# Performance work log

Hardware: AMD Instinct MI355X
Metric: run time of the kernel (lower is better)

## Reference

```python
import jax, jax.numpy as jnp
import numpy as np

B, T, H, V = 16, 400, 400, 22000
S, STEPS, NG = 30, 8, 3  # n_slots, max_res_len, n_gates


def setup_inputs() -> dict:
    key = jax.random.key(0)
    ks = jax.random.split(key, 12)
    r = lambda k, shape, s: jax.random.normal(k, shape, jnp.float32) * s
    lens = jnp.sort(jax.random.randint(ks[8], (B,), T // 2, T + 1))[::-1]
    lens = lens.at[0].set(T)  # torch code only masks up to max(lens); make max(lens)==T
    return {
        "embedding": r(ks[0], (V, H), 0.1),
        "gru_Wih": r(ks[1], (3 * H, H), 0.05),
        "gru_Whh": r(ks[2], (3 * H, H), 0.05),
        "gru_bih": jnp.zeros((3 * H,), jnp.float32),
        "gru_bhh": jnp.zeros((3 * H,), jnp.float32),
        "W_ratio": r(ks[3], (1, 3 * H), 0.05),
        "b_ratio": jnp.zeros((1,), jnp.float32),
        "W_gate": r(ks[4], (NG, H), 0.05),
        "b_gate": jnp.zeros((NG,), jnp.float32),
        "slot_embs": r(ks[5], (S, H), 0.1),  # domain_emb + slot_emb, precombined per domain-slot
        "encoded_hidden": r(ks[6], (B, H), 1.0),
        "encoded_outputs": r(ks[7], (B, T, H), 1.0),
        "encoded_lens": lens,
        "story": jax.random.randint(ks[9], (B, T), 0, V),
        "target_batches": jax.random.randint(ks[10], (B, S, STEPS), 0, V),
    }


def reference(embedding, gru_Wih, gru_Whh, gru_bih, gru_bhh, W_ratio, b_ratio,
              W_gate, b_gate, slot_embs, encoded_hidden, encoded_outputs,
              encoded_lens, story, target_batches):
    # dropout is identity at eval; use_teacher_forcing=True.
    mask = jnp.arange(T)[None, :] < encoded_lens[:, None]          # [B, T]
    batch_idx = jnp.arange(B)[:, None]

    def gru_cell(x, h):
        gi = x @ gru_Wih.T + gru_bih                                # [B, 3H]
        gh = h @ gru_Whh.T + gru_bhh
        i_r, i_z, i_n = jnp.split(gi, 3, axis=-1)
        h_r, h_z, h_n = jnp.split(gh, 3, axis=-1)
        r = jax.nn.sigmoid(i_r + h_r)
        z = jax.nn.sigmoid(i_z + h_z)
        n = jnp.tanh(i_n + r * h_n)
        return (1.0 - z) * n + z * h

    def per_slot(slot_emb, tgt_steps):  # slot_emb [H], tgt_steps [STEPS, B]
        dec_in0 = jnp.broadcast_to(slot_emb[None, :], (B, H))

        def step(carry, tgt_w):
            h, dec_in = carry
            h = gru_cell(dec_in, h)                                 # dec_state == new hidden
            logits = jnp.einsum('bth,bh->bt', encoded_outputs, h)   # [B, T]
            attn = jax.nn.softmax(jnp.where(mask, logits, -1e9), axis=1)
            context = jnp.einsum('bt,bth->bh', attn, encoded_outputs)
            p_vocab = jax.nn.softmax(h @ embedding.T, axis=1)       # [B, V]
            pg_in = jnp.concatenate([h, context, dec_in], axis=-1)  # [B, 3H]
            p_gen = jax.nn.sigmoid(pg_in @ W_ratio.T + b_ratio)     # [B, 1]
            p_ctx = jnp.zeros((B, V), p_vocab.dtype).at[batch_idx, story].add(attn)
            p_final = (1.0 - p_gen) * p_ctx + p_gen * p_vocab       # [B, V]
            dec_next = embedding[tgt_w]                             # teacher forcing
            return (h, dec_next), (p_final, context)

        _, (points, contexts) = jax.lax.scan(step, (encoded_hidden, dec_in0), tgt_steps)
        gate = contexts[0] @ W_gate.T + b_gate                      # gate uses step-0 context
        return jnp.transpose(points, (1, 0, 2)), gate               # [B, STEPS, V], [B, NG]

    targets = jnp.transpose(target_batches, (1, 2, 0))              # [S, STEPS, B]
    all_point_outputs, all_gate_outputs = jax.vmap(per_slot)(slot_embs, targets)
    return all_point_outputs, all_gate_outputs  # [S,B,STEPS,V], [S,B,NG]
```

## Files before the change

### kernel.cpp

```cpp
#include <hip/hip_runtime.h>
#include <hip/hip_bf16.h>

#define DEV __device__ __forceinline__

constexpr int B = 16, T = 400, H = 400, V = 22000, S = 30, STEPS = 8, NG = 3;
constexpr int M  = S * B;
constexpr int H3 = 3 * H;
constexpr int KP = 416;
constexpr int VP = 22016;
constexpr int MP = 512;
constexpr int MR = STEPS * MP;
constexpr int NWP = 1280;
constexpr int NBLK = VP / 128;
constexpr int NMP = MR / 256;
constexpr int NVB = NBLK * NMP;
constexpr int NVB_S = NBLK * 2;
constexpr int NCT = (H3 + 63) / 64;
constexpr int NGH = NCT * ((M + 63) / 64);
constexpr int TPAD = 416;
constexpr int PLD = 424;
constexpr long long PTS = (long long)S * B * STEPS * V;

typedef __attribute__((ext_vector_type(8))) short bfrag;
typedef __attribute__((ext_vector_type(4))) float f32x4;
typedef unsigned short u16;

DEV u16 f2bf(float x) {
  unsigned u = __float_as_uint(x);
  u += 0x7FFFu + ((u >> 16) & 1u);
  return (u16)(u >> 16);
}
DEV u16 f2bfn(float x) {
  __hip_bfloat16 h = __float2bfloat16(x);
  union { __hip_bfloat16 b; u16 u; } cv; cv.b = h; return cv.u;
}
DEV float bf2f(u16 h) { return __uint_as_float(((unsigned)h) << 16); }
DEV float sigm(float x) { return 1.0f / (1.0f + __expf(-x)); }

DEV void gload16(const u16* g, u16* l) {
  __builtin_amdgcn_global_load_lds(
      (const __attribute__((address_space(1))) void*)g,
      (__attribute__((address_space(3))) void*)l, 16, 0, 0);
}

constexpr int N_EMB = VP * KP / 256;
constexpr int N_ENC = B * 400 * TPAD / 256;
constexpr int N_W   = NWP * KP / 256;
constexpr int N_DEC = STEPS * MP * KP / 256;
constexpr int N_H0  = MP * KP / 256;
constexpr int N_ZP  = STEPS * (MP - M) * KP / 256;
constexpr int N_ZE  = MR * 16 / 256;
constexpr int N_INIT = N_EMB + N_ENC + N_W + N_DEC + N_H0 + N_ZP + N_ZE;

__global__ __launch_bounds__(256) void k_init(
    const float* __restrict__ emb, const float* __restrict__ enc,
    const float* __restrict__ Wih, const float* __restrict__ Whh,
    const float* __restrict__ semb, const float* __restrict__ ehid,
    const int* __restrict__ tgt,
    u16* __restrict__ ebf, u16* __restrict__ encbK, u16* __restrict__ encT,
    u16* __restrict__ wihH, u16* __restrict__ wihL,
    u16* __restrict__ whhH, u16* __restrict__ whhL,
    float* __restrict__ dec, u16* __restrict__ decH, u16* __restrict__ decL,
    float* __restrict__ h0F, u16* __restrict__ h0H, u16* __restrict__ h0L,
    u16* __restrict__ hAllH, u16* __restrict__ hAllL, u16* __restrict__ ebuf)
{
  int bx = blockIdx.x;
  const int tid = threadIdx.x;
  if (bx < N_EMB) {
    int i = bx * 256 + tid;
    int v = i / KP, k = i % KP;
    ebf[i] = f2bf((v < V && k < H) ? emb[(long long)v * H + k] : 0.f);
    return;
  }
  bx -= N_EMB;
  if (bx < N_ENC) {
    int i = bx * 256 + tid;
    int c = i % TPAD, r = (i / TPAD) % 400, b = i / (TPAD * 400);
    encbK[i] = f2bf((c < H) ? enc[((size_t)b * T + r) * H + c] : 0.f);
    encT[i]  = f2bf((c < T) ? enc[((size_t)b * T + c) * H + r] : 0.f);
    return;
  }
  bx -= N_ENC;
  if (bx < N_W) {
    int i = bx * 256 + tid;
    int n = i / KP, k = i % KP;
    float v1 = (n < H3 && k < H) ? Wih[n * H + k] : 0.f;
    u16 h1 = f2bf(v1);
    wihH[i] = h1; wihL[i] = f2bf(v1 - bf2f(h1));
    float v2 = (n < H3 && k < H) ? Whh[n * H + k] : 0.f;
    u16 h2 = f2bf(v2);
    whhH[i] = h2; whhL[i] = f2bf(v2 - bf2f(h2));
    return;
  }
  bx -= N_W;
  if (bx < N_DEC) {
    int i = bx * 256 + tid;
    int k = i % KP, m = (i / KP) % MP, s = i / (KP * MP);
    float val = 0.f;
    if (m < M && k < H) {
      int slot = m / B, b = m % B;
      if (s == 0) val = semb[slot * H + k];
      else        val = emb[(long long)tgt[(b * S + slot) * STEPS + (s - 1)] * H + k];
      dec[((long long)s * M + m) * H + k] = val;
    }
    u16 hi = f2bf(val);
    decH[i] = hi; decL[i] = f2bf(val - bf2f(hi));
    return;
  }
  bx -= N_DEC;
  if (bx < N_H0) {
    int i = bx * 256 + tid;
    int k = i % KP, m = i / KP;
    float val = (m < M && k < H) ? ehid[(m % B) * H + k] : 0.f;
    if (m < M && k < H) h0F[m * H + k] = val;
    u16 hi = f2bf(val);
    h0H[i] = hi; h0L[i] = f2bf(val - bf2f(hi));
    return;
  }
  bx -= N_H0;
  if (bx < N_ZP) {
    int i = bx * 256 + tid;
    int k = i % KP;
    int row = M + (i / KP) % (MP - M);
    int s = i / (KP * (MP - M));
    size_t idx = ((size_t)s * MP + row) * KP + k;
    hAllH[idx] = 0; hAllL[idx] = 0;
    return;
  }
  bx -= N_ZP;
  {
    int i = bx * 256 + tid;
    int row = i / 16, col = V + (i % 16);
    ebuf[(size_t)row * VP + col] = 0;
  }
}

__global__ __launch_bounds__(256) void k_gemm64s(
    const u16* __restrict__ Ahi, const u16* __restrict__ Alo,
    const u16* __restrict__ Bmh, const u16* __restrict__ Bml,
    const float* __restrict__ bias, float* __restrict__ C,
    int Mvalid, int Nvalid, int Cstride)
{
  __shared__ u16 BsH[64 * 32], BsL[64 * 32];
  const int tid = threadIdx.x;
  const int wave = tid >> 6, lane = tid & 63;
  const int wm = wave >> 1, wn = wave & 1;
  const int n0 = blockIdx.x * 64;
  const int m0 = blockIdx.y * 64;
  const int lrow = lane & 15;
  const int c16 = lane >> 4;
  const int srow = tid >> 2;
  const int sg = (tid & 3) ^ (srow & 3);
  f32x4 acc[2][2] = {};

  const u16* aH = Ahi + (size_t)(m0 + wm * 32 + lrow) * KP + c16 * 8;
  const u16* aL = Alo + (size_t)(m0 + wm * 32 + lrow) * KP + c16 * 8;
  const u16* bHs = Bmh + (size_t)(n0 + srow) * KP + sg * 8;
  const u16* bLs = Bml + (size_t)(n0 + srow) * KP + sg * 8;
  u16* lBH = BsH + wave * 512;
  u16* lBL = BsL + wave * 512;

  for (int kk = 0; kk < KP / 32; ++kk) {
    const int kb = kk * 32;
    gload16(bHs + kb, lBH);
    gload16(bLs + kb, lBL);
    __syncthreads();
    bfrag a0h = *(const bfrag*)(aH + kb);
    bfrag a1h = *(const bfrag*)(aH + 16 * KP + kb);
    bfrag a0l = *(const bfrag*)(aL + kb);
    bfrag a1l = *(const bfrag*)(aL + 16 * KP + kb);
#pragma unroll
    for (int nn = 0; nn < 2; ++nn) {
      const int br = wn * 32 + nn * 16 + lrow;
      const int goff = br * 32 + ((c16 ^ (br & 3)) << 3);
      bfrag bh = *(const bfrag*)&BsH[goff];
      bfrag bl = *(const bfrag*)&BsL[goff];
      acc[0][nn] = __builtin_amdgcn_mfma_f32_16x16x32_bf16(a0h, bh, acc[0][nn], 0, 0, 0);
      acc[1][nn] = __builtin_amdgcn_mfma_f32_16x16x32_bf16(a1h, bh, acc[1][nn], 0, 0, 0);
      acc[0][nn] = __builtin_amdgcn_mfma_f32_16x16x32_bf16(a0h, bl, acc[0][nn], 0, 0, 0);
      acc[1][nn] = __builtin_amdgcn_mfma_f32_16x16x32_bf16(a1h, bl, acc[1][nn], 0, 0, 0);
      acc[0][nn] = __builtin_amdgcn_mfma_f32_16x16x32_bf16(a0l, bh, acc[0][nn], 0, 0, 0);
      acc[1][nn] = __builtin_amdgcn_mfma_f32_16x16x32_bf16(a1l, bh, acc[1][nn], 0, 0, 0);
    }
    __syncthreads();
  }
  const int orow = (lane >> 4) << 2, ocol = lane & 15;
#pragma unroll
  for (int am = 0; am < 2; ++am) {
#pragma unroll
    for (int nn = 0; nn < 2; ++nn) {
      const int gn = n0 + wn * 32 + nn * 16 + ocol;
      if (gn >= Nvalid) continue;
      const float badd = bias[gn];
#pragma unroll
      for (int r = 0; r < 4; ++r) {
        const int gm = m0 + wm * 32 + am * 16 + orow + r;
        if (gm < Mvalid) C[(long long)gm * Cstride + gn] = acc[am][nn][r] + badd;
      }
    }
  }
}

__global__ __launch_bounds__(512) void k_cell(const float* __restrict__ gi_s,
                                              const float* __restrict__ gh,
                                              const float* __restrict__ hprevF,
                                              float* __restrict__ hcurF,
                                              u16* __restrict__ hHc, u16* __restrict__ hLc) {
  int i = blockIdx.x * 512 + threadIdx.x;
  if (i >= M * H) return;
  int k = i % H, m = i / H;
  float ir = gi_s[m * H3 + k],         hr = gh[m * H3 + k];
  float iz = gi_s[m * H3 + H + k],     hz = gh[m * H3 + H + k];
  float in_ = gi_s[m * H3 + 2*H + k],  hn = gh[m * H3 + 2*H + k];
  float rr = sigm(ir + hr);
  float z = sigm(iz + hz);
  float n = tanhf(in_ + rr * hn);
  float hv = (1.f - z) * n + z * hprevF[i];
  hcurF[i] = hv;
  u16 hb = f2bf(hv);
  hHc[m * KP + k] = hb;
  hLc[m * KP + k] = f2bf(hv - bf2f(hb));
}

__global__ __launch_bounds__(512) void k_bigv(
    const u16* __restrict__ hPrevH, const u16* __restrict__ hPrevL,
    const u16* __restrict__ ebf, u16* __restrict__ ebuf, long long Rbase,
    const u16* __restrict__ whhH, const u16* __restrict__ whhL,
    const float* __restrict__ bhh, float* __restrict__ gh)
{
  __shared__ union SMU {
    u16 vb[4][4096];
    struct { u16 bh[64 * 32]; u16 bl[64 * 32]; } g;
  } sm;
  const int bx = blockIdx.x;
  const int tid = threadIdx.x;
  const int wave = tid >> 6, lane = tid & 63;

  if (bx < NVB_S) {
    const int bxs = (bx & 7) * (NVB_S / 8) + (bx >> 3);
    const int nb = bxs >> 1;
    const int m0 = (bxs & 1) * 256;
    const int n0 = nb * 128;
    const int wm = wave >> 1, wn = wave & 1;
    const int lrow = lane & 15;
    const int c16 = lane >> 4;
    const int srow = tid >> 2;
    const int sg = (tid & 3) ^ (srow & 3);
    f32x4 acc[4][4] = {};

    const u16* aBase = hPrevH + (size_t)(m0 + wm * 64 + lrow) * KP + c16 * 8;
    const u16* bS = ebf + (size_t)(n0 + srow) * KP + sg * 8;

    gload16(bS + 0,  &sm.vb[0][wave * 512]);
    gload16(bS + 32, &sm.vb[1][wave * 512]);
    int cur = 0;
#pragma unroll 1
    for (int p = 0; p < 7; ++p) {
      const int kb = p * 64;
      bfrag a[4][2];
#pragma unroll
      for (int r = 0; r < 4; ++r) {
        a[r][0] = *(const bfrag*)(aBase + r * 16 * KP + kb);
        if (p < 6) a[r][1] = *(const bfrag*)(aBase + r * 16 * KP + kb + 32);
      }
      if (p < 5) {
        gload16(bS + kb + 64, &sm.vb[(cur ^ 1) * 2 + 0][wave * 512]);
        gload16(bS + kb + 96, &sm.vb[(cur ^ 1) * 2 + 1][wave * 512]);
        asm volatile("s_waitcnt vmcnt(10)" ::: "memory");
      } else if (p == 5) {
        gload16(bS + kb + 64, &sm.vb[(cur ^ 1) * 2 + 0][wave * 512]);
        asm volatile("s_waitcnt vmcnt(9)" ::: "memory");
      } else {
        asm volatile("s_waitcnt vmcnt(4)" ::: "memory");
      }
      __builtin_amdgcn_sched_barrier(0);
      __builtin_amdgcn_s_barrier();
      {
        const u16* Bb = sm.vb[cur * 2 + 0];
        bfrag bfv[4];
#pragma unroll
        for (int nn = 0; nn < 4; ++nn) {
          const int brr = wn * 64 + nn * 16 + lrow;
          bfv[nn] = *(const bfrag*)&Bb[brr * 32 + ((c16 ^ (brr & 3)) << 3)];
        }
#pragma unroll
        for (int nn = 0; nn < 4; ++nn) {
#pragma unroll
          for (int r = 0; r < 4; ++r)
            acc[r][nn] = __builtin_amdgcn_mfma_f32_16x16x32_bf16(a[r][0], bfv[nn], acc[r][nn], 0, 0, 0);
        }
      }
      if (p < 6) {
        const u16* Bb = sm.vb[cur * 2 + 1];
        bfrag bfv[4];
#pragma unroll
        for (int nn = 0; nn < 4; ++nn) {
          const int brr = wn * 64 + nn * 16 + lrow;
          bfv[nn] = *(const bfrag*)&Bb[brr * 32 + ((c16 ^ (brr & 3)) << 3)];
        }
#pragma unroll
        for (int nn = 0; nn < 4; ++nn) {
#pragma unroll
          for (int r = 0; r < 4; ++r)
            acc[r][nn] = __builtin_amdgcn_mfma_f32_16x16x32_bf16(a[r][1], bfv[nn], acc[r][nn], 0, 0, 0);
        }
      }
      __builtin_amdgcn_sched_barrier(0);
      __builtin_amdgcn_s_barrier();
      __builtin_amdgcn_sched_barrier(0);
      cur ^= 1;
    }

    const int orow = (lane >> 4) << 2, ocol = lane & 15;
#pragma unroll
    for (int af = 0; af < 4; ++af) {
#pragma unroll
      for (int r = 0; r < 4; ++r) {
        const int rl = m0 + wm * 64 + af * 16 + orow + r;
        if (rl >= M) continue;
        const size_t R = (size_t)(Rbase + rl);
#pragma unroll
        for (int nn = 0; nn < 4; ++nn) {
          const int gn = n0 + wn * 64 + nn * 16 + ocol;
          if (gn < V) ebuf[R * VP + gn] = f2bfn(__expf(acc[af][nn][r]));
        }
      }
    }
  } else {
    const int gb = bx - NVB_S;
    const int n0 = (gb % NCT) * 64;
    const int m0 = (gb / NCT) * 64;
    const bool act = tid < 256;
    const int wm = wave >> 1, wn = wave & 1;
    const int lrow = lane & 15;
    const int c16 = lane >> 4;
    const int srow = tid >> 2;
    const int sg = (tid & 3) ^ (srow & 3);
    f32x4 acc[2][2] = {};

    const u16* aH = hPrevH + (size_t)(m0 + (wm & 1) * 32 + lrow) * KP + c16 * 8;
    const u16* aL = hPrevL + (size_t)(m0 + (wm & 1) * 32 + lrow) * KP + c16 * 8;
    const u16* bHs = whhH + (size_t)(n0 + (srow & 63)) * KP + sg * 8;
    const u16* bLs = whhL + (size_t)(n0 + (srow & 63)) * KP + sg * 8;
    u16* lBH = sm.g.bh + (wave & 3) * 512;
    u16* lBL = sm.g.bl + (wave & 3) * 512;

    for (int kk = 0; kk < KP / 32; ++kk) {
      const int kb = kk * 32;
      if (act) {
        gload16(bHs + kb, lBH);
        gload16(bLs + kb, lBL);
      }
      __syncthreads();
      if (act) {
        bfrag a0h = *(const bfrag*)(aH + kb);
        bfrag a1h = *(const bfrag*)(aH + 16 * KP + kb);
        bfrag a0l = *(const bfrag*)(aL + kb);
        bfrag a1l = *(const bfrag*)(aL + 16 * KP + kb);
#pragma unroll
        for (int nn = 0; nn < 2; ++nn) {
          const int br = wn * 32 + nn * 16 + lrow;
          const int goff = br * 32 + ((c16 ^ (br & 3)) << 3);
          bfrag bh = *(const bfrag*)&sm.g.bh[goff];
          bfrag bl = *(const bfrag*)&sm.g.bl[goff];
          acc[0][nn] = __builtin_amdgcn_mfma_f32_16x16x32_bf16(a0h, bh, acc[0][nn], 0, 0, 0);
          acc[1][nn] = __builtin_amdgcn_mfma_f32_16x16x32_bf16(a1h, bh, acc[1][nn], 0, 0, 0);
          acc[0][nn] = __builtin_amdgcn_mfma_f32_16x16x32_bf16(a0h, bl, acc[0][nn], 0, 0, 0);
          acc[1][nn] = __builtin_amdgcn_mfma_f32_16x16x32_bf16(a1h, bl, acc[1][nn], 0, 0, 0);
          acc[0][nn] = __builtin_amdgcn_mfma_f32_16x16x32_bf16(a0l, bh, acc[0][nn], 0, 0, 0);
          acc[1][nn] = __builtin_amdgcn_mfma_f32_16x16x32_bf16(a1l, bh, acc[1][nn], 0, 0, 0);
        }
      }
      __syncthreads();
    }
    if (act) {
      const int orow = (lane >> 4) << 2, ocol = lane & 15;
#pragma unroll
      for (int am = 0; am < 2; ++am) {
#pragma unroll
        for (int nn = 0; nn < 2; ++nn) {
          const int gn = n0 + wn * 32 + nn * 16 + ocol;
          if (gn >= H3) continue;
          const float badd = bhh[gn];
#pragma unroll
          for (int r = 0; r < 4; ++r) {
            const int gm = m0 + wm * 32 + am * 16 + orow + r;
            if (gm < M) gh[(long long)gm * H3 + gn] = acc[am][nn][r] + badd;
          }
        }
      }
    }
  }
}

struct SMatt {
  u16 P[32 * PLD];
  float partm[32][4];
  float parts[32][4];
  float rowred[32];
  float part2[32][4][4];
};

__global__ __launch_bounds__(512) void k_attn(
    const u16* __restrict__ hAllH, const u16* __restrict__ hAllL,
    const float* __restrict__ hallF,
    const u16* __restrict__ encbK, const u16* __restrict__ encT,
    const int* __restrict__ lens, const float* __restrict__ dec,
    const float* __restrict__ Wr, const float* __restrict__ br,
    const float* __restrict__ Wg, const float* __restrict__ bg,
    float* __restrict__ attnB, float* __restrict__ pgenB, float* __restrict__ out)
{
  __shared__ SMatt sm;
  const int s = blockIdx.x >> 4;
  const int b = blockIdx.x & 15;
  const int tid = threadIdx.x;
  const int wave = tid >> 6, lane = tid & 63;
  const int mt = wave & 1;
  const int wg = wave >> 1;
  const int lrow = lane & 15;
  const int c16 = lane >> 4;
  const int len = lens[b];
  const int rbase = mt * 16 + c16 * 4;

  for (int idx = tid; idx < 32 * 24; idx += 512)
    sm.P[(idx / 24) * PLD + 400 + (idx % 24)] = 0;

  f32x4 acc[7] = {};
  {
    const size_t arow = (size_t)s * MP + (size_t)(mt * 16 + lrow) * B + b;
    const u16* aHp = hAllH + arow * KP + c16 * 8;
    const u16* aLp = hAllL + arow * KP + c16 * 8;
    const u16* bBase = encbK + (size_t)b * 400 * TPAD + c16 * 8;
    for (int kk = 0; kk < 13; ++kk) {
      bfrag ah = *(const bfrag*)(aHp + kk * 32);
      bfrag al = *(const bfrag*)(aLp + kk * 32);
#pragma unroll
      for (int i = 0; i < 7; ++i) {
        const int jt = wg + 4 * i;
        if (jt < 25) {
          bfrag bv = *(const bfrag*)(bBase + (size_t)(jt * 16 + lrow) * TPAD + kk * 32);
          acc[i] = __builtin_amdgcn_mfma_f32_16x16x32_bf16(ah, bv, acc[i], 0, 0, 0);
          acc[i] = __builtin_amdgcn_mfma_f32_16x16x32_bf16(al, bv, acc[i], 0, 0, 0);
        }
      }
    }
  }

  {
    float pm[4] = {-1e30f, -1e30f, -1e30f, -1e30f};
#pragma unroll
    for (int i = 0; i < 7; ++i) {
      const int jt = wg + 4 * i;
      if (jt >= 25) continue;
      const int t = jt * 16 + lrow;
      const bool ok = t < len;
#pragma unroll
      for (int rr = 0; rr < 4; ++rr) pm[rr] = fmaxf(pm[rr], ok ? acc[i][rr] : -1e30f);
    }
#pragma unroll
    for (int d = 1; d < 16; d <<= 1) {
#pragma unroll
      for (int rr = 0; rr < 4; ++rr) pm[rr] = fmaxf(pm[rr], __shfl_xor(pm[rr], d));
    }
    if (lrow == 0) {
#pragma unroll
      for (int rr = 0; rr < 4; ++rr) sm.partm[rbase + rr][wg] = pm[rr];
    }
  }
  __syncthreads();
  if (tid < 32)
    sm.rowred[tid] = fmaxf(fmaxf(sm.partm[tid][0], sm.partm[tid][1]),
                           fmaxf(sm.partm[tid][2], sm.partm[tid][3]));
  __syncthreads();
  float Mx[4];
#pragma unroll
  for (int rr = 0; rr < 4; ++rr) Mx[rr] = sm.rowred[rbase + rr];
  {
    float ps[4] = {0.f, 0.f, 0.f, 0.f};
#pragma unroll
    for (int i = 0; i < 7; ++i) {
      const int jt = wg + 4 * i;
      if (jt >= 25) continue;
      const int t = jt * 16 + lrow;
      const bool ok = t < len;
#pragma unroll
      for (int rr = 0; rr < 4; ++rr) {
        float e = ok ? __expf(acc[i][rr] - Mx[rr]) : 0.f;
        acc[i][rr] = e;
        ps[rr] += e;
      }
    }
#pragma unroll
    for (int d = 1; d < 16; d <<= 1) {
#pragma unroll
      for (int rr = 0; rr < 4; ++rr) ps[rr] += __shfl_xor(ps[rr], d);
    }
    if (lrow == 0) {
#pragma unroll
      for (int rr = 0; rr < 4; ++rr) sm.parts[rbase + rr][wg] = ps[rr];
    }
  }
  __syncthreads();
  if (tid < 32)
    sm.rowred[tid] = sm.parts[tid][0] + sm.parts[tid][1] + sm.parts[tid][2] + sm.parts[tid][3];
  __syncthreads();
  {
    float inv[4];
#pragma unroll
    for (int rr = 0; rr < 4; ++rr) inv[rr] = 1.f / sm.rowred[rbase + rr];
#pragma unroll
    for (int i = 0; i < 7; ++i) {
      const int jt = wg + 4 * i;
      if (jt >= 25) continue;
      const int t = jt * 16 + lrow;
#pragma unroll
      for (int rr = 0; rr < 4; ++rr) {
        const int row = rbase + rr;
        const float p = acc[i][rr] * inv[rr];
        sm.P[row * PLD + t] = f2bfn(p);
        if (row < 30) attnB[((size_t)s * M + row * B + b) * T + t] = p;
      }
    }
  }
  __syncthreads();

  f32x4 acc2[7] = {};
  {
    const u16* bBase = encT + (size_t)b * 400 * TPAD + c16 * 8;
    const u16* aP = sm.P + (mt * 16 + lrow) * PLD + c16 * 8;
    for (int kk = 0; kk < 13; ++kk) {
      bfrag ap = *(const bfrag*)(aP + kk * 32);
#pragma unroll
      for (int i = 0; i < 7; ++i) {
        const int jk = wg + 4 * i;
        if (jk < 25) {
          bfrag bv = *(const bfrag*)(bBase + (size_t)(jk * 16 + lrow) * TPAD + kk * 32);
          acc2[i] = __builtin_amdgcn_mfma_f32_16x16x32_bf16(ap, bv, acc2[i], 0, 0, 0);
        }
      }
    }
  }
  {
    float pw[4] = {0.f, 0.f, 0.f, 0.f};
    float pg0[4] = {0.f, 0.f, 0.f, 0.f};
    float pg1[4] = {0.f, 0.f, 0.f, 0.f};
    float pg2[4] = {0.f, 0.f, 0.f, 0.f};
    const bool do_g = (s == 0);
#pragma unroll
    for (int i = 0; i < 7; ++i) {
      const int jk = wg + 4 * i;
      if (jk >= 25) continue;
      const int k = jk * 16 + lrow;
      const float wr = Wr[H + k];
      float w0 = 0.f, w1 = 0.f, w2 = 0.f;
      if (do_g) { w0 = Wg[k]; w1 = Wg[H + k]; w2 = Wg[2 * H + k]; }
#pragma unroll
      for (int rr = 0; rr < 4; ++rr) {
        const float v = acc2[i][rr];
        pw[rr] = fmaf(v, wr, pw[rr]);
        if (do_g) {
          pg0[rr] = fmaf(v, w0, pg0[rr]);
          pg1[rr] = fmaf(v, w1, pg1[rr]);
          pg2[rr] = fmaf(v, w2, pg2[rr]);
        }
      }
    }
#pragma unroll
    for (int d = 1; d < 16; d <<= 1) {
#pragma unroll
      for (int rr = 0; rr < 4; ++rr) {
        pw[rr] += __shfl_xor(pw[rr], d);
        pg0[rr] += __shfl_xor(pg0[rr], d);
        pg1[rr] += __shfl_xor(pg1[rr], d);
        pg2[rr] += __shfl_xor(pg2[rr], d);
      }
    }
    if (lrow == 0) {
#pragma unroll
      for (int rr = 0; rr < 4; ++rr) {
        sm.part2[rbase + rr][wg][0] = pw[rr];
        sm.part2[rbase + rr][wg][1] = pg0[rr];
        sm.part2[rbase + rr][wg][2] = pg1[rr];
        sm.part2[rbase + rr][wg][3] = pg2[rr];
      }
    }
  }
  __syncthreads();

  if (tid < 480) {
    const int row = tid >> 4;
    const int l16 = tid & 15;
    const int m = row * B + b;
    const float* hF = hallF + ((size_t)s * M + m) * H;
    const float* dF = dec + ((size_t)s * M + m) * H;
    float p = 0.f;
    for (int j = 0; j < 25; ++j) {
      const int k = l16 + 16 * j;
      p += hF[k] * Wr[k] + dF[k] * Wr[2 * H + k];
    }
#pragma unroll
    for (int d = 1; d < 16; d <<= 1) p += __shfl_xor(p, d);
    if (l16 == 0) {
      float cw = sm.part2[row][0][0] + sm.part2[row][1][0] +
                 sm.part2[row][2][0] + sm.part2[row][3][0];
      pgenB[s * M + m] = sigm(p + cw + br[0]);
    }
    if (s == 0 && l16 < NG) {
      float gv = sm.part2[row][0][1 + l16] + sm.part2[row][1][1 + l16] +
                 sm.part2[row][2][1 + l16] + sm.part2[row][3][1 + l16];
      out[PTS + (long long)m * NG + l16] = gv + bg[l16];
    }
  }
}

__global__ __launch_bounds__(512) void k_merge(
    const u16* __restrict__ ebuf, const float* __restrict__ pgenB,
    const float* __restrict__ attnB, const int* __restrict__ story,
    float* __restrict__ out)
{
  const int bxi = blockIdx.x;
  const int s = bxi / M, m = bxi % M, b = m % B;
  const size_t R = (size_t)s * MP + m;
  const int tid = threadIdx.x;
  const int wave = tid >> 6, lane = tid & 63;
  __shared__ float red8[8];
  const u16* erow = ebuf + R * VP;
  bfrag ch[6];
  float sum = 0.f;
#pragma unroll
  for (int j = 0; j < 6; ++j) {
    const int c = j * 512 + tid;
    if (c < VP / 8) {
      ch[j] = *(const bfrag*)(erow + (size_t)c * 8);
#pragma unroll
      for (int e = 0; e < 8; ++e) sum += bf2f((u16)ch[j][e]);
    }
  }
#pragma unroll
  for (int off = 32; off; off >>= 1) sum += __shfl_xor(sum, off);
  if (lane == 0) red8[wave] = sum;
  __syncthreads();
  float Sv = 0.f;
#pragma unroll
  for (int j = 0; j < 8; ++j) Sv += red8[j];
  const float pg = pgenB[s * M + m];
  const float scale = pg / Sv;
  float* orow = out + ((size_t)m * STEPS + s) * V;
#pragma unroll
  for (int j = 0; j < 6; ++j) {
    const int c = j * 512 + tid;
    if (c < V / 8) {
      f32x4 w0, w1;
#pragma unroll
      for (int e = 0; e < 4; ++e) {
        w0[e] = bf2f((u16)ch[j][e]) * scale;
        w1[e] = bf2f((u16)ch[j][4 + e]) * scale;
      }
      *(f32x4*)(orow + (size_t)c * 8) = w0;
      *(f32x4*)(orow + (size_t)c * 8 + 4) = w1;
    }
  }
  __syncthreads();
  const float om = 1.f - pg;
  for (int t = tid; t < T; t += 512) {
    float a = attnB[((size_t)s * M + m) * T + t];
    if (a != 0.f) atomicAdd(orow + story[b * T + t], om * a);
  }
}


extern "C" void kernel_launch(void* const* d_in, const int* in_sizes, int n_in,
                              void* d_out, int out_size, void* d_ws, size_t ws_size,
                              hipStream_t stream) {
  (void)in_sizes; (void)n_in; (void)out_size; (void)ws_size;
  const float* emb  = (const float*)d_in[0];
  const float* Wih  = (const float*)d_in[1];
  const float* Whh  = (const float*)d_in[2];
  const float* bih  = (const float*)d_in[3];
  const float* bhh  = (const float*)d_in[4];
  const float* Wr   = (const float*)d_in[5];
  const float* br   = (const float*)d_in[6];
  const float* Wg   = (const float*)d_in[7];
  const float* bg   = (const float*)d_in[8];
  const float* semb = (const float*)d_in[9];
  const float* ehid = (const float*)d_in[10];
  const float* enc  = (const float*)d_in[11];
  const int*   lens = (const int*)d_in[12];
  const int*   story= (const int*)d_in[13];
  const int*   tgt  = (const int*)d_in[14];
  float* out = (float*)d_out;

  char* w = (char*)d_ws;
  size_t off = 0;
  auto alloc = [&](size_t n) -> void* {
    void* p = w + off;
    off = (off + n + 255) & ~(size_t)255;
    return p;
  };
  u16* ebf    = (u16*)alloc((size_t)VP * KP * 2);
  u16* wihH   = (u16*)alloc((size_t)NWP * KP * 2);
  u16* wihL   = (u16*)alloc((size_t)NWP * KP * 2);
  u16* whhH   = (u16*)alloc((size_t)NWP * KP * 2);
  u16* whhL   = (u16*)alloc((size_t)NWP * KP * 2);
  u16* decH   = (u16*)alloc((size_t)STEPS * MP * KP * 2);
  u16* decL   = (u16*)alloc((size_t)STEPS * MP * KP * 2);
  float* dec  = (float*)alloc((size_t)STEPS * M * H * 4);
  float* h0F  = (float*)alloc((size_t)M * H * 4);
  u16* h0H    = (u16*)alloc((size_t)MP * KP * 2);
  u16* h0L    = (u16*)alloc((size_t)MP * KP * 2);
  u16* hAllH  = (u16*)alloc((size_t)MR * KP * 2);
  u16* hAllL  = (u16*)alloc((size_t)MR * KP * 2);
  float* hallF= (float*)alloc((size_t)STEPS * M * H * 4);
  float* gi   = (float*)alloc((size_t)MR * H3 * 4);
  float* gh   = (float*)alloc((size_t)M * H3 * 4);
  float* attnB= (float*)alloc((size_t)STEPS * M * T * 4);
  float* pgenB= (float*)alloc((size_t)STEPS * M * 4);
  u16* ebuf   = (u16*)alloc((size_t)MR * VP * 2);
  u16* encbK  = (u16*)alloc((size_t)B * 400 * TPAD * 2);
  u16* encT   = (u16*)alloc((size_t)B * 400 * TPAD * 2);

  k_init<<<N_INIT, 256, 0, stream>>>(emb, enc, Wih, Whh, semb, ehid, tgt,
      ebf, encbK, encT, wihH, wihL, whhH, whhL, dec, decH, decL,
      h0F, h0H, h0L, hAllH, hAllL, ebuf);
  k_gemm64s<<<dim3(NCT, MR / 64), 256, 0, stream>>>(
      decH, decL, wihH, wihL, bih, gi, MR, H3, H3);

  k_gemm64s<<<dim3(NCT, (M + 63) / 64), 256, 0, stream>>>(
      h0H, h0L, whhH, whhL, bhh, gh, M, H3, H3);
  k_cell<<<(M * H + 511) / 512, 512, 0, stream>>>(
      gi, gh, h0F, hallF, hAllH, hAllL);

  for (int s = 1; s < STEPS; ++s) {
    k_bigv<<<NVB_S + NGH, 512, 0, stream>>>(
        hAllH + (size_t)(s - 1) * MP * KP, hAllL + (size_t)(s - 1) * MP * KP,
        ebf, ebuf, (long long)(s - 1) * MP, whhH, whhL, bhh, gh);
    k_cell<<<(M * H + 511) / 512, 512, 0, stream>>>(
        gi + (size_t)s * MP * H3, gh, hallF + (size_t)(s - 1) * M * H,
        hallF + (size_t)s * M * H,
        hAllH + (size_t)s * MP * KP, hAllL + (size_t)s * MP * KP);
  }
  k_bigv<<<NVB_S, 512, 0, stream>>>(
      hAllH + (size_t)7 * MP * KP, hAllL + (size_t)7 * MP * KP,
      ebf, ebuf, (long long)7 * MP, whhH, whhL, bhh, gh);

  k_attn<<<STEPS * B, 512, 0, stream>>>(hAllH, hAllL, hallF, encbK, encT, lens,
                                        dec, Wr, br, Wg, bg, attnB, pgenB, out);
  k_merge<<<STEPS * M, 512, 0, stream>>>(ebuf, pgenB, attnB, story, out);
}
```

Before: 554.5 us.

## Fuse attention and merge stages into per-step vocab/GH kernel as software pipeline

Folds the attention and merge kernels into the per-step k_bigv launch. Each launch now runs block ranges for the vocab GEMM at step s-1, the Whh GEMM at step s, attention at step s-1 and merge at step s-2, with negative indices disabling a role. The aim is to let the small attention and merge work fill idle CUs beside the per-step GEMMs instead of running as separate tail launches. In exchange the fused kernel needs more registers and a larger shared-memory union, which may lower occupancy for the vocab GEMM blocks, and one extra launch is added at the end to drain the pipeline.

```diff
diff --git a/kernel.cpp b/kernel.cpp
--- a/kernel.cpp
+++ b/kernel.cpp
@@ -12,11 +12,14 @@
 constexpr int MR = STEPS * MP;
 constexpr int NWP = 1280;
 constexpr int NBLK = VP / 128;
-constexpr int NMP = MR / 256;
-constexpr int NVB = NBLK * NMP;
 constexpr int NVB_S = NBLK * 2;
 constexpr int NCT = (H3 + 63) / 64;
 constexpr int NGH = NCT * ((M + 63) / 64);
+constexpr int GB_VOC = 0;
+constexpr int GB_GH  = NVB_S;
+constexpr int GB_ATT = GB_GH + NGH;
+constexpr int GB_MRG = GB_ATT + B;
+constexpr int GB_ALL = GB_MRG + M;
 constexpr int TPAD = 416;
 constexpr int PLD = 424;
 constexpr long long PTS = (long long)S * B * STEPS * V;
@@ -222,21 +225,42 @@
   hLc[m * KP + k] = f2bf(hv - bf2f(hb));
 }
 
+struct SMatt {
+  u16 P[32 * PLD];
+  float partm[32][4];
+  float parts[32][4];
+  float rowred[32];
+  float part2[32][4][4];
+};
+
 __global__ __launch_bounds__(512) void k_bigv(
-    const u16* __restrict__ hPrevH, const u16* __restrict__ hPrevL,
-    const u16* __restrict__ ebf, u16* __restrict__ ebuf, long long Rbase,
+    const u16* __restrict__ hAllH, const u16* __restrict__ hAllL,
+    const float* __restrict__ hallF,
+    const u16* __restrict__ ebf, u16* __restrict__ ebuf,
     const u16* __restrict__ whhH, const u16* __restrict__ whhL,
-    const float* __restrict__ bhh, float* __restrict__ gh)
+    const float* __restrict__ bhh, float* __restrict__ gh,
+    const u16* __restrict__ encbK, const u16* __restrict__ encT,
+    const int* __restrict__ lens, const float* __restrict__ dec,
+    const float* __restrict__ Wr, const float* __restrict__ br,
+    const float* __restrict__ Wg, const float* __restrict__ bg,
+    float* __restrict__ attnB, float* __restrict__ pgenB,
+    const int* __restrict__ story, float* __restrict__ out,
+    int vS, int ghS, int aS, int mS)
 {
   __shared__ union SMU {
     u16 vb[4][4096];
     struct { u16 bh[64 * 32]; u16 bl[64 * 32]; } g;
+    SMatt a;
+    float red8[8];
   } sm;
   const int bx = blockIdx.x;
   const int tid = threadIdx.x;
   const int wave = tid >> 6, lane = tid & 63;
 
-  if (bx < NVB_S) {
+  if (bx < GB_GH) {
+    if (vS < 0) return;
+    const u16* hPrevH = hAllH + (size_t)vS * MP * KP;
+    const long long Rbase = (long long)vS * MP;
     const int bxs = (bx & 7) * (NVB_S / 8) + (bx >> 3);
     const int nb = bxs >> 1;
     const int m0 = (bxs & 1) * 256;
@@ -326,8 +350,11 @@
         }
       }
     }
-  } else {
-    const int gb = bx - NVB_S;
+  } else if (bx < GB_ATT) {
+    if (ghS < 0) return;
+    const u16* hPrevH = hAllH + (size_t)(ghS - 1) * MP * KP;
+    const u16* hPrevL = hAllL + (size_t)(ghS - 1) * MP * KP;
+    const int gb = bx - GB_GH;
     const int n0 = (gb % NCT) * 64;
     const int m0 = (gb / NCT) * 64;
     const bool act = tid < 256;
@@ -390,281 +417,254 @@
         }
       }
     }
-  }
-}
-
-struct SMatt {
-  u16 P[32 * PLD];
-  float partm[32][4];
-  float parts[32][4];
-  float rowred[32];
-  float part2[32][4][4];
-};
-
-__global__ __launch_bounds__(512) void k_attn(
-    const u16* __restrict__ hAllH, const u16* __restrict__ hAllL,
-    const float* __restrict__ hallF,
-    const u16* __restrict__ encbK, const u16* __restrict__ encT,
-    const int* __restrict__ lens, const float* __restrict__ dec,
-    const float* __restrict__ Wr, const float* __restrict__ br,
-    const float* __restrict__ Wg, const float* __restrict__ bg,
-    float* __restrict__ attnB, float* __restrict__ pgenB, float* __restrict__ out)
-{
-  __shared__ SMatt sm;
-  const int s = blockIdx.x >> 4;
-  const int b = blockIdx.x & 15;
-  const int tid = threadIdx.x;
-  const int wave = tid >> 6, lane = tid & 63;
-  const int mt = wave & 1;
-  const int wg = wave >> 1;
-  const int lrow = lane & 15;
-  const int c16 = lane >> 4;
-  const int len = lens[b];
-  const int rbase = mt * 16 + c16 * 4;
-
-  for (int idx = tid; idx < 32 * 24; idx += 512)
-    sm.P[(idx / 24) * PLD + 400 + (idx % 24)] = 0;
-
-  f32x4 acc[7] = {};
-  {
-    const size_t arow = (size_t)s * MP + (size_t)(mt * 16 + lrow) * B + b;
-    const u16* aHp = hAllH + arow * KP + c16 * 8;
-    const u16* aLp = hAllL + arow * KP + c16 * 8;
-    const u16* bBase = encbK + (size_t)b * 400 * TPAD + c16 * 8;
-    for (int kk = 0; kk < 13; ++kk) {
-      bfrag ah = *(const bfrag*)(aHp + kk * 32);
-      bfrag al = *(const bfrag*)(aLp + kk * 32);
+  } else if (bx < GB_MRG) {
+    if (aS < 0) return;
+    const int s = aS;
+    const int b = bx - GB_ATT;
+    const int mt = wave & 1;
+    const int wg = wave >> 1;
+    const int lrow = lane & 15;
+    const int c16 = lane >> 4;
+    const int len = lens[b];
+    const int rbase = mt * 16 + c16 * 4;
+
+    for (int idx = tid; idx < 32 * 24; idx += 512)
+      sm.a.P[(idx / 24) * PLD + 400 + (idx % 24)] = 0;
+
+    f32x4 acc[7] = {};
+    {
+      const size_t arow = (size_t)s * MP + (size_t)(mt * 16 + lrow) * B + b;
+      const u16* aHp = hAllH + arow * KP + c16 * 8;
+      const u16* aLp = hAllL + arow * KP + c16 * 8;
+      const u16* bBase = encbK + (size_t)b * 400 * TPAD + c16 * 8;
+      for (int kk = 0; kk < 13; ++kk) {
+        bfrag ah = *(const bfrag*)(aHp + kk * 32);
+        bfrag al = *(const bfrag*)(aLp + kk * 32);
+#pragma unroll
+        for (int i = 0; i < 7; ++i) {
+          const int jt = wg + 4 * i;
+          if (jt < 25) {
+            bfrag bv = *(const bfrag*)(bBase + (size_t)(jt * 16 + lrow) * TPAD + kk * 32);
+            acc[i] = __builtin_amdgcn_mfma_f32_16x16x32_bf16(ah, bv, acc[i], 0, 0, 0);
+            acc[i] = __builtin_amdgcn_mfma_f32_16x16x32_bf16(al, bv, acc[i], 0, 0, 0);
+          }
+        }
+      }
+    }
+
+    {
+      float pm[4] = {-1e30f, -1e30f, -1e30f, -1e30f};
 #pragma unroll
       for (int i = 0; i < 7; ++i) {
         const int jt = wg + 4 * i;
-        if (jt < 25) {
-          bfrag bv = *(const bfrag*)(bBase + (size_t)(jt * 16 + lrow) * TPAD + kk * 32);
-          acc[i] = __builtin_amdgcn_mfma_f32_16x16x32_bf16(ah, bv, acc[i], 0, 0, 0);
-          acc[i] = __builtin_amdgcn_mfma_f32_16x16x32_bf16(al, bv, acc[i], 0, 0, 0);
-        }
-      }
-    }
-  }
-
-  {
-    float pm[4] = {-1e30f, -1e30f, -1e30f, -1e30f};
-#pragma unroll
-    for (int i = 0; i < 7; ++i) {
-      const int jt = wg + 4 * i;
-      if (jt >= 25) continue;
-      const int t = jt * 16 + lrow;
-      const bool ok = t < len;
-#pragma unroll
-      for (int rr = 0; rr < 4; ++rr) pm[rr] = fmaxf(pm[rr], ok ? acc[i][rr] : -1e30f);
-    }
-#pragma unroll
-    for (int d = 1; d < 16; d <<= 1) {
-#pragma unroll
-      for (int rr = 0; rr < 4; ++rr) pm[rr] = fmaxf(pm[rr], __shfl_xor(pm[rr], d));
-    }
-    if (lrow == 0) {
-#pragma unroll
-      for (int rr = 0; rr < 4; ++rr) sm.partm[rbase + rr][wg] = pm[rr];
-    }
-  }
-  __syncthreads();
-  if (tid < 32)
-    sm.rowred[tid] = fmaxf(fmaxf(sm.partm[tid][0], sm.partm[tid][1]),
-                           fmaxf(sm.partm[tid][2], sm.partm[tid][3]));
-  __syncthreads();
-  float Mx[4];
-#pragma unroll
-  for (int rr = 0; rr < 4; ++rr) Mx[rr] = sm.rowred[rbase + rr];
-  {
-    float ps[4] = {0.f, 0.f, 0.f, 0.f};
-#pragma unroll
-    for (int i = 0; i < 7; ++i) {
-      const int jt = wg + 4 * i;
-      if (jt >= 25) continue;
-      const int t = jt * 16 + lrow;
-      const bool ok = t < len;
-#pragma unroll
-      for (int rr = 0; rr < 4; ++rr) {
-        float e = ok ? __expf(acc[i][rr] - Mx[rr]) : 0.f;
-        acc[i][rr] = e;
-        ps[rr] += e;
-      }
-    }
-#pragma unroll
-    for (int d = 1; d < 16; d <<= 1) {
-#pragma unroll
-      for (int rr = 0; rr < 4; ++rr) ps[rr] += __shfl_xor(ps[rr], d);
-    }
-    if (lrow == 0) {
-#pragma unroll
-      for (int rr = 0; rr < 4; ++rr) sm.parts[rbase + rr][wg] = ps[rr];
-    }
-  }
-  __syncthreads();
-  if (tid < 32)
-    sm.rowred[tid] = sm.parts[tid][0] + sm.parts[tid][1] + sm.parts[tid][2] + sm.parts[tid][3];
-  __syncthreads();
-  {
-    float inv[4];
-#pragma unroll
-    for (int rr = 0; rr < 4; ++rr) inv[rr] = 1.f / sm.rowred[rbase + rr];
-#pragma unroll
-    for (int i = 0; i < 7; ++i) {
-      const int jt = wg + 4 * i;
-      if (jt >= 25) continue;
-      const int t = jt * 16 + lrow;
-#pragma unroll
-      for (int rr = 0; rr < 4; ++rr) {
-        const int row = rbase + rr;
-        const float p = acc[i][rr] * inv[rr];
-        sm.P[row * PLD + t] = f2bfn(p);
-        if (row < 30) attnB[((size_t)s * M + row * B + b) * T + t] = p;
-      }
-    }
-  }
-  __syncthreads();
-
-  f32x4 acc2[7] = {};
-  {
-    const u16* bBase = encT + (size_t)b * 400 * TPAD + c16 * 8;
-    const u16* aP = sm.P + (mt * 16 + lrow) * PLD + c16 * 8;
-    for (int kk = 0; kk < 13; ++kk) {
-      bfrag ap = *(const bfrag*)(aP + kk * 32);
+        if (jt >= 25) continue;
+        const int t = jt * 16 + lrow;
+        const bool ok = t < len;
+#pragma unroll
+        for (int rr = 0; rr < 4; ++rr) pm[rr] = fmaxf(pm[rr], ok ? acc[i][rr] : -1e30f);
+      }
+#pragma unroll
+      for (int d = 1; d < 16; d <<= 1) {
+#pragma unroll
+        for (int rr = 0; rr < 4; ++rr) pm[rr] = fmaxf(pm[rr], __shfl_xor(pm[rr], d));
+      }
+      if (lrow == 0) {
+#pragma unroll
+        for (int rr = 0; rr < 4; ++rr) sm.a.partm[rbase + rr][wg] = pm[rr];
+      }
+    }
+    __syncthreads();
+    if (tid < 32)
+      sm.a.rowred[tid] = fmaxf(fmaxf(sm.a.partm[tid][0], sm.a.partm[tid][1]),
+                               fmaxf(sm.a.partm[tid][2], sm.a.partm[tid][3]));
+    __syncthreads();
+    float Mx[4];
+#pragma unroll
+    for (int rr = 0; rr < 4; ++rr) Mx[rr] = sm.a.rowred[rbase + rr];
+    {
+      float ps[4] = {0.f, 0.f, 0.f, 0.f};
+#pragma unroll
+      for (int i = 0; i < 7; ++i) {
+        const int jt = wg + 4 * i;
+        if (jt >= 25) continue;
+        const int t = jt * 16 + lrow;
+        const bool ok = t < len;
+#pragma unroll
+        for (int rr = 0; rr < 4; ++rr) {
+          float e = ok ? __expf(acc[i][rr] - Mx[rr]) : 0.f;
+          acc[i][rr] = e;
+          ps[rr] += e;
+        }
+      }
+#pragma unroll
+      for (int d = 1; d < 16; d <<= 1) {
+#pragma unroll
+        for (int rr = 0; rr < 4; ++rr) ps[rr] += __shfl_xor(ps[rr], d);
+      }
+      if (lrow == 0) {
+#pragma unroll
+        for (int rr = 0; rr < 4; ++rr) sm.a.parts[rbase + rr][wg] = ps[rr];
+      }
+    }
+    __syncthreads();
+    if (tid < 32)
+      sm.a.rowred[tid] = sm.a.parts[tid][0] + sm.a.parts[tid][1] + sm.a.parts[tid][2] + sm.a.parts[tid][3];
+    __syncthreads();
+    {
+      float inv[4];
+#pragma unroll
+      for (int rr = 0; rr < 4; ++rr) inv[rr] = 1.f / sm.a.rowred[rbase + rr];
+#pragma unroll
+      for (int i = 0; i < 7; ++i) {
+        const int jt = wg + 4 * i;
+        if (jt >= 25) continue;
+        const int t = jt * 16 + lrow;
+#pragma unroll
+        for (int rr = 0; rr < 4; ++rr) {
+          const int row = rbase + rr;
+          const float p = acc[i][rr] * inv[rr];
+          sm.a.P[row * PLD + t] = f2bfn(p);
+          if (row < 30) attnB[((size_t)s * M + row * B + b) * T + t] = p;
+        }
+      }
+    }
+    __syncthreads();
+
+    f32x4 acc2[7] = {};
+    {
+      const u16* bBase = encT + (size_t)b * 400 * TPAD + c16 * 8;
+      const u16* aP = sm.a.P + (mt * 16 + lrow) * PLD + c16 * 8;
+      for (int kk = 0; kk < 13; ++kk) {
+        bfrag ap = *(const bfrag*)(aP + kk * 32);
+#pragma unroll
+        for (int i = 0; i < 7; ++i) {
+          const int jk = wg + 4 * i;
+          if (jk < 25) {
+            bfrag bv = *(const bfrag*)(bBase + (size_t)(jk * 16 + lrow) * TPAD + kk * 32);
+            acc2[i] = __builtin_amdgcn_mfma_f32_16x16x32_bf16(ap, bv, acc2[i], 0, 0, 0);
+          }
+        }
+      }
+    }
+    {
+      float pw[4] = {0.f, 0.f, 0.f, 0.f};
+      float pg0[4] = {0.f, 0.f, 0.f, 0.f};
+      float pg1[4] = {0.f, 0.f, 0.f, 0.f};
+      float pg2[4] = {0.f, 0.f, 0.f, 0.f};
+      const bool do_g = (s == 0);
 #pragma unroll
       for (int i = 0; i < 7; ++i) {
         const int jk = wg + 4 * i;
-        if (jk < 25) {
-          bfrag bv = *(const bfrag*)(bBase + (size_t)(jk * 16 + lrow) * TPAD + kk * 32);
-          acc2[i] = __builtin_amdgcn_mfma_f32_16x16x32_bf16(ap, bv, acc2[i], 0, 0, 0);
-        }
-      }
-    }
-  }
-  {
-    float pw[4] = {0.f, 0.f, 0.f, 0.f};
-    float pg0[4] = {0.f, 0.f, 0.f, 0.f};
-    float pg1[4] = {0.f, 0.f, 0.f, 0.f};
-    float pg2[4] = {0.f, 0.f, 0.f, 0.f};
-    const bool do_g = (s == 0);
-#pragma unroll
-    for (int i = 0; i < 7; ++i) {
-      const int jk = wg + 4 * i;
-      if (jk >= 25) continue;
-      const int k = jk * 16 + lrow;
-      const float wr = Wr[H + k];
-      float w0 = 0.f, w1 = 0.f, w2 = 0.f;
-      if (do_g) { w0 = Wg[k]; w1 = Wg[H + k]; w2 = Wg[2 * H + k]; }
-#pragma unroll
-      for (int rr = 0; rr < 4; ++rr) {
-        const float v = acc2[i][rr];
-        pw[rr] = fmaf(v, wr, pw[rr]);
-        if (do_g) {
-          pg0[rr] = fmaf(v, w0, pg0[rr]);
-          pg1[rr] = fmaf(v, w1, pg1[rr]);
-          pg2[rr] = fmaf(v, w2, pg2[rr]);
-        }
-      }
-    }
-#pragma unroll
-    for (int d = 1; d < 16; d <<= 1) {
-#pragma unroll
-      for (int rr = 0; rr < 4; ++rr) {
-        pw[rr] += __shfl_xor(pw[rr], d);
-        pg0[rr] += __shfl_xor(pg0[rr], d);
-        pg1[rr] += __shfl_xor(pg1[rr], d);
-        pg2[rr] += __shfl_xor(pg2[rr], d);
-      }
-    }
-    if (lrow == 0) {
-#pragma unroll
-      for (int rr = 0; rr < 4; ++rr) {
-        sm.part2[rbase + rr][wg][0] = pw[rr];
-        sm.part2[rbase + rr][wg][1] = pg0[rr];
-        sm.part2[rbase + rr][wg][2] = pg1[rr];
-        sm.part2[rbase + rr][wg][3] = pg2[rr];
-      }
-    }
-  }
-  __syncthreads();
-
-  if (tid < 480) {
-    const int row = tid >> 4;
-    const int l16 = tid & 15;
-    const int m = row * B + b;
-    const float* hF = hallF + ((size_t)s * M + m) * H;
-    const float* dF = dec + ((size_t)s * M + m) * H;
-    float p = 0.f;
-    for (int j = 0; j < 25; ++j) {
-      const int k = l16 + 16 * j;
-      p += hF[k] * Wr[k] + dF[k] * Wr[2 * H + k];
-    }
-#pragma unroll
-    for (int d = 1; d < 16; d <<= 1) p += __shfl_xor(p, d);
-    if (l16 == 0) {
-      float cw = sm.part2[row][0][0] + sm.part2[row][1][0] +
-                 sm.part2[row][2][0] + sm.part2[row][3][0];
-      pgenB[s * M + m] = sigm(p + cw + br[0]);
-    }
-    if (s == 0 && l16 < NG) {
-      float gv = sm.part2[row][0][1 + l16] + sm.part2[row][1][1 + l16] +
-                 sm.part2[row][2][1 + l16] + sm.part2[row][3][1 + l16];
-      out[PTS + (long long)m * NG + l16] = gv + bg[l16];
-    }
-  }
-}
-
-__global__ __launch_bounds__(512) void k_merge(
-    const u16* __restrict__ ebuf, const float* __restrict__ pgenB,
-    const float* __restrict__ attnB, const int* __restrict__ story,
-    float* __restrict__ out)
-{
-  const int bxi = blockIdx.x;
-  const int s = bxi / M, m = bxi % M, b = m % B;
-  const size_t R = (size_t)s * MP + m;
-  const int tid = threadIdx.x;
-  const int wave = tid >> 6, lane = tid & 63;
-  __shared__ float red8[8];
-  const u16* erow = ebuf + R * VP;
-  bfrag ch[6];
-  float sum = 0.f;
-#pragma unroll
-  for (int j = 0; j < 6; ++j) {
-    const int c = j * 512 + tid;
-    if (c < VP / 8) {
-      ch[j] = *(const bfrag*)(erow + (size_t)c * 8);
-#pragma unroll
-      for (int e = 0; e < 8; ++e) sum += bf2f((u16)ch[j][e]);
-    }
-  }
-#pragma unroll
-  for (int off = 32; off; off >>= 1) sum += __shfl_xor(sum, off);
-  if (lane == 0) red8[wave] = sum;
-  __syncthreads();
-  float Sv = 0.f;
-#pragma unroll
-  for (int j = 0; j < 8; ++j) Sv += red8[j];
-  const float pg = pgenB[s * M + m];
-  const float scale = pg / Sv;
-  float* orow = out + ((size_t)m * STEPS + s) * V;
-#pragma unroll
-  for (int j = 0; j < 6; ++j) {
-    const int c = j * 512 + tid;
-    if (c < V / 8) {
-      f32x4 w0, w1;
-#pragma unroll
-      for (int e = 0; e < 4; ++e) {
-        w0[e] = bf2f((u16)ch[j][e]) * scale;
-        w1[e] = bf2f((u16)ch[j][4 + e]) * scale;
-      }
-      *(f32x4*)(orow + (size_t)c * 8) = w0;
-      *(f32x4*)(orow + (size_t)c * 8 + 4) = w1;
-    }
-  }
-  __syncthreads();
-  const float om = 1.f - pg;
-  for (int t = tid; t < T; t += 512) {
-    float a = attnB[((size_t)s * M + m) * T + t];
-    if (a != 0.f) atomicAdd(orow + story[b * T + t], om * a);
+        if (jk >= 25) continue;
+        const int k = jk * 16 + lrow;
+        const float wr = Wr[H + k];
+        float w0 = 0.f, w1 = 0.f, w2 = 0.f;
+        if (do_g) { w0 = Wg[k]; w1 = Wg[H + k]; w2 = Wg[2 * H + k]; }
+#pragma unroll
+        for (int rr = 0; rr < 4; ++rr) {
+          const float v = acc2[i][rr];
+          pw[rr] = fmaf(v, wr, pw[rr]);
+          if (do_g) {
+            pg0[rr] = fmaf(v, w0, pg0[rr]);
+            pg1[rr] = fmaf(v, w1, pg1[rr]);
+            pg2[rr] = fmaf(v, w2, pg2[rr]);
+          }
+        }
+      }
+#pragma unroll
+      for (int d = 1; d < 16; d <<= 1) {
+#pragma unroll
+        for (int rr = 0; rr < 4; ++rr) {
+          pw[rr] += __shfl_xor(pw[rr], d);
+          pg0[rr] += __shfl_xor(pg0[rr], d);
+          pg1[rr] += __shfl_xor(pg1[rr], d);
+          pg2[rr] += __shfl_xor(pg2[rr], d);
+        }
+      }
+      if (lrow == 0) {
+#pragma unroll
+        for (int rr = 0; rr < 4; ++rr) {
+          sm.a.part2[rbase + rr][wg][0] = pw[rr];
+          sm.a.part2[rbase + rr][wg][1] = pg0[rr];
+          sm.a.part2[rbase + rr][wg][2] = pg1[rr];
+          sm.a.part2[rbase + rr][wg][3] = pg2[rr];
+        }
+      }
+    }
+    __syncthreads();
+
+    if (tid < 480) {
+      const int row = tid >> 4;
+      const int l16 = tid & 15;
+      const int m = row * B + b;
+      const float* hF = hallF + ((size_t)s * M + m) * H;
+      const float* dF = dec + ((size_t)s * M + m) * H;
+      float p = 0.f;
+      for (int j = 0; j < 25; ++j) {
+        const int k = l16 + 16 * j;
+        p += hF[k] * Wr[k] + dF[k] * Wr[2 * H + k];
+      }
+#pragma unroll
+      for (int d = 1; d < 16; d <<= 1) p += __shfl_xor(p, d);
+      if (l16 == 0) {
+        float cw = sm.a.part2[row][0][0] + sm.a.part2[row][1][0] +
+                   sm.a.part2[row][2][0] + sm.a.part2[row][3][0];
+        pgenB[s * M + m] = sigm(p + cw + br[0]);
+      }
+      if (s == 0 && l16 < NG) {
+        float gv = sm.a.part2[row][0][1 + l16] + sm.a.part2[row][1][1 + l16] +
+                   sm.a.part2[row][2][1 + l16] + sm.a.part2[row][3][1 + l16];
+        out[PTS + (long long)m * NG + l16] = gv + bg[l16];
+      }
+    }
+  } else {
+    if (mS < 0) return;
+    const int s = mS;
+    const int m = bx - GB_MRG;
+    const int b = m % B;
+    const size_t R = (size_t)s * MP + m;
+    const u16* erow = ebuf + R * VP;
+    bfrag ch[6];
+    float sum = 0.f;
+#pragma unroll
+    for (int j = 0; j < 6; ++j) {
+      const int c = j * 512 + tid;
+      if (c < VP / 8) {
+        ch[j] = *(const bfrag*)(erow + (size_t)c * 8);
+#pragma unroll
+        for (int e = 0; e < 8; ++e) sum += bf2f((u16)ch[j][e]);
+      }
+    }
+#pragma unroll
+    for (int off = 32; off; off >>= 1) sum += __shfl_xor(sum, off);
+    if (lane == 0) sm.red8[wave] = sum;
+    __syncthreads();
+    float Sv = 0.f;
+#pragma unroll
+    for (int j = 0; j < 8; ++j) Sv += sm.red8[j];
+    const float pg = pgenB[s * M + m];
+    const float scale = pg / Sv;
+    float* orow = out + ((size_t)m * STEPS + s) * V;
+#pragma unroll
+    for (int j = 0; j < 6; ++j) {
+      const int c = j * 512 + tid;
+      if (c < V / 8) {
+        f32x4 w0, w1;
+#pragma unroll
+        for (int e = 0; e < 4; ++e) {
+          w0[e] = bf2f((u16)ch[j][e]) * scale;
+          w1[e] = bf2f((u16)ch[j][4 + e]) * scale;
+        }
+        *(f32x4*)(orow + (size_t)c * 8) = w0;
+        *(f32x4*)(orow + (size_t)c * 8 + 4) = w1;
+      }
+    }
+    __syncthreads();
+    const float om = 1.f - pg;
+    for (int t = tid; t < T; t += 512) {
+      float a = attnB[((size_t)s * M + m) * T + t];
+      if (a != 0.f) atomicAdd(orow + story[b * T + t], om * a);
+    }
   }
 }
 
@@ -731,19 +731,21 @@
       gi, gh, h0F, hallF, hAllH, hAllL);
 
   for (int s = 1; s < STEPS; ++s) {
-    k_bigv<<<NVB_S + NGH, 512, 0, stream>>>(
-        hAllH + (size_t)(s - 1) * MP * KP, hAllL + (size_t)(s - 1) * MP * KP,
-        ebf, ebuf, (long long)(s - 1) * MP, whhH, whhL, bhh, gh);
+    k_bigv<<<GB_ALL, 512, 0, stream>>>(
+        hAllH, hAllL, hallF, ebf, ebuf, whhH, whhL, bhh, gh,
+        encbK, encT, lens, dec, Wr, br, Wg, bg, attnB, pgenB, story, out,
+        s - 1, s, s - 1, s - 2);
     k_cell<<<(M * H + 511) / 512, 512, 0, stream>>>(
         gi + (size_t)s * MP * H3, gh, hallF + (size_t)(s - 1) * M * H,
         hallF + (size_t)s * M * H,
         hAllH + (size_t)s * MP * KP, hAllL + (size_t)s * MP * KP);
   }
-  k_bigv<<<NVB_S, 512, 0, stream>>>(
-      hAllH + (size_t)7 * MP * KP, hAllL + (size_t)7 * MP * KP,
-      ebf, ebuf, (long long)7 * MP, whhH, whhL, bhh, gh);
-
-  k_attn<<<STEPS * B, 512, 0, stream>>>(hAllH, hAllL, hallF, encbK, encT, lens,
-                                        dec, Wr, br, Wg, bg, attnB, pgenB, out);
-  k_merge<<<STEPS * M, 512, 0, stream>>>(ebuf, pgenB, attnB, story, out);
+  k_bigv<<<GB_ALL, 512, 0, stream>>>(
+      hAllH, hAllL, hallF, ebf, ebuf, whhH, whhL, bhh, gh,
+      encbK, encT, lens, dec, Wr, br, Wg, bg, attnB, pgenB, story, out,
+      7, -1, 7, 6);
+  k_bigv<<<GB_ALL, 512, 0, stream>>>(
+      hAllH, hAllL, hallF, ebf, ebuf, whhH, whhL, bhh, gh,
+      encbK, encT, lens, dec, Wr, br, Wg, bg, attnB, pgenB, story, out,
+      -1, -1, -1, 7);
 }
```

After: 731.6 us. 31.9% more time.
